# Performance work log

Measured on AMD Instinct MI355X. Metric: run time of the kernel, lower is better.

## Reference

```python
import jax, jax.numpy as jnp
import numpy as np

RBF_START = 0.0
RBF_END = 8.0
RBF_STEPS = 32
OUT_SIZE = 64
ENERGY_SCALE = 0.01


def setup_inputs() -> dict:
    key = jax.random.key(0)
    k1, k2, k3, k4 = jax.random.split(key, 4)
    L, R = 512, 4096
    return {
        "lig_feat": jax.random.normal(k1, (L, RBF_STEPS, OUT_SIZE), dtype=jnp.float32),
        "rec_feat": jax.random.normal(k2, (R, RBF_STEPS, OUT_SIZE), dtype=jnp.float32),
        "lig_coord": jax.random.normal(k3, (L, 3), dtype=jnp.float32),
        "rec_coord": jax.random.normal(k4, (R, 3), dtype=jnp.float32),
    }


def reference(lig_feat, rec_feat, lig_coord, rec_coord):
    # attention coefficients: contract over (rbf step 'e' kept, feature 'f' summed)
    atn_coefs = jnp.einsum('lef,ref->lre', lig_feat, rec_feat)  # [L,R,steps]
    # pairwise distances [L,R]
    diff = lig_coord[:, None, :] - rec_coord[None, :, :]
    dists = jnp.sqrt(jnp.sum(diff * diff, axis=-1))
    # RBF encoding [L,R,steps]
    mu = jnp.linspace(RBF_START, RBF_END, RBF_STEPS, dtype=dists.dtype)
    sigma = (RBF_START - RBF_END) / RBF_STEPS
    z = (dists[..., None] - mu) / sigma
    rbfs = jnp.exp(-(z * z))
    # weighted energy sum (scalar)
    U = jnp.sum(atn_coefs * rbfs) * ENERGY_SCALE
    return U
```

## Files before the change

### kernel.cpp

```cpp
#include <hip/hip_runtime.h>
#include <math.h>

#define LN 512
#define RN 4096
#define EN 32
#define FN 64

#define BLT 128
#define BRT 128
#define EH  8

#define K16LOG2E 23.083120654223415f
#define MU_STEP (8.0f / 31.0f)

typedef _Float16 half8 __attribute__((ext_vector_type(8)));
typedef __attribute__((ext_vector_type(4))) float f32x4;

#define APLANE 0
#define BPLANE (128 * 128)
#define LDS_BYTES (2 * 128 * 128)

__global__ __launch_bounds__(512, 1) void ff_mfma(
    const float* __restrict__ lig_feat,
    const float* __restrict__ rec_feat,
    const float* __restrict__ lig_coord,
    const float* __restrict__ rec_coord,
    float* __restrict__ partial)
{
    extern __shared__ char lds[];

    const int tid  = threadIdx.x;
    const int lane = tid & 63;
    const int w    = tid >> 6;
    const int wl   = (w & 3) * 2;
    const int wr   = (w >> 2) * 4;
    const int lrow = lane & 15;
    const int lk   = lane >> 4;

    const int l0 = blockIdx.y * BLT;
    const int r0 = blockIdx.x * BRT;
    const int e0 = blockIdx.z * EH;

    float rcx[4], rcy[4], rcz[4];
    #pragma unroll
    for (int tj = 0; tj < 4; ++tj) {
        const int r = r0 + (wr + tj) * 16 + lrow;
        rcx[tj] = rec_coord[r * 3 + 0];
        rcy[tj] = rec_coord[r * 3 + 1];
        rcz[tj] = rec_coord[r * 3 + 2];
    }
    float d[2][4][4];
    #pragma unroll
    for (int ti = 0; ti < 2; ++ti) {
        #pragma unroll
        for (int i = 0; i < 4; ++i) {
            const int l = l0 + (wl + ti) * 16 + lk * 4 + i;
            const float lx = lig_coord[l * 3 + 0];
            const float ly = lig_coord[l * 3 + 1];
            const float lz = lig_coord[l * 3 + 2];
            #pragma unroll
            for (int tj = 0; tj < 4; ++tj) {
                const float dx = lx - rcx[tj];
                const float dy = ly - rcy[tj];
                const float dz = lz - rcz[tj];
                d[ti][tj][i] = sqrtf(fmaf(dx, dx, fmaf(dy, dy, dz * dz)));
            }
        }
    }

    float usum = 0.0f;

    for (int ee = 0; ee < EH; ++ee) {
        const int e = e0 + ee;

        __syncthreads();

        #pragma unroll
        for (int k = 0; k < 8; ++k) {
            const int idx = k * 512 + tid;
            const int row = (idx >> 4) & 127;
            const int c   = idx & 15;
            const float4 v = (k < 4)
                ? *(const float4*)&lig_feat[((l0 + row) * EN + e) * FN + c * 4]
                : *(const float4*)&rec_feat[((r0 + row) * EN + e) * FN + c * 4];

            const unsigned short h0 = __builtin_bit_cast(unsigned short, (_Float16)v.x);
            const unsigned short h1 = __builtin_bit_cast(unsigned short, (_Float16)v.y);
            const unsigned short h2 = __builtin_bit_cast(unsigned short, (_Float16)v.z);
            const unsigned short h3 = __builtin_bit_cast(unsigned short, (_Float16)v.w);
            uint2 hw;
            hw.x = (unsigned)h0 | ((unsigned)h1 << 16);
            hw.y = (unsigned)h2 | ((unsigned)h3 << 16);

            const int off = row * 128 + ((c * 8) ^ ((row & 7) << 4));
            *(uint2*)(lds + ((k < 4) ? APLANE : BPLANE) + off) = hw;
        }
        __syncthreads();

        f32x4 acc[2][4];
        #pragma unroll
        for (int ti = 0; ti < 2; ++ti)
            #pragma unroll
            for (int tj = 0; tj < 4; ++tj)
                acc[ti][tj] = (f32x4){0.f, 0.f, 0.f, 0.f};

        #pragma unroll
        for (int kc = 0; kc < 2; ++kc) {
            const int inrow = (kc * 64 + lk * 16) ^ ((lrow & 7) << 4);
            half8 af[2], bf_[4];
            #pragma unroll
            for (int t = 0; t < 2; ++t) {
                const int arow = (wl + t) * 16 + lrow;
                af[t] = *(const half8*)(lds + APLANE + arow * 128 + inrow);
            }
            #pragma unroll
            for (int t = 0; t < 4; ++t) {
                const int brow = (wr + t) * 16 + lrow;
                bf_[t] = *(const half8*)(lds + BPLANE + brow * 128 + inrow);
            }
            #pragma unroll
            for (int ti = 0; ti < 2; ++ti) {
                #pragma unroll
                for (int tj = 0; tj < 4; ++tj) {
                    acc[ti][tj] = __builtin_amdgcn_mfma_f32_16x16x32_f16(
                        af[ti], bf_[tj], acc[ti][tj], 0, 0, 0);
                }
            }
        }

        const float mu = (float)e * MU_STEP;
        #pragma unroll
        for (int ti = 0; ti < 2; ++ti) {
            #pragma unroll
            for (int tj = 0; tj < 4; ++tj) {
                #pragma unroll
                for (int i = 0; i < 4; ++i) {
                    const float t = d[ti][tj][i] - mu;
                    const float wgt = __builtin_amdgcn_exp2f(-K16LOG2E * t * t);
                    usum = fmaf(acc[ti][tj][i], wgt, usum);
                }
            }
        }
    }

    __syncthreads();
    float* red = (float*)lds;
    red[tid] = usum;
    __syncthreads();
    #pragma unroll
    for (int st = 256; st > 0; st >>= 1) {
        if (tid < st) red[tid] += red[tid + st];
        __syncthreads();
    }
    if (tid == 0) {
        const int bidx = (blockIdx.z * gridDim.y + blockIdx.y) * gridDim.x + blockIdx.x;
        partial[bidx] = red[0];
    }
}

__global__ __launch_bounds__(256) void ff_reduce(
    const float* __restrict__ partial, float* __restrict__ out, int n)
{
    __shared__ float s[256];
    float v = 0.0f;
    for (int i = threadIdx.x; i < n; i += 256) v += partial[i];
    s[threadIdx.x] = v;
    __syncthreads();
    #pragma unroll
    for (int st = 128; st > 0; st >>= 1) {
        if (threadIdx.x < st) s[threadIdx.x] += s[threadIdx.x + st];
        __syncthreads();
    }
    if (threadIdx.x == 0) out[0] = s[0] * 0.01f;
}

extern "C" void kernel_launch(void* const* d_in, const int* in_sizes, int n_in,
                              void* d_out, int out_size, void* d_ws, size_t ws_size,
                              hipStream_t stream)
{
    const float* lig_feat  = (const float*)d_in[0];
    const float* rec_feat  = (const float*)d_in[1];
    const float* lig_coord = (const float*)d_in[2];
    const float* rec_coord = (const float*)d_in[3];
    float* out = (float*)d_out;
    float* partial = (float*)d_ws;

    const dim3 grid(RN / BRT, LN / BLT, EN / EH);
    ff_mfma<<<grid, dim3(512), LDS_BYTES, stream>>>(
        lig_feat, rec_feat, lig_coord, rec_coord, partial);

    const int nPartial = (RN / BRT) * (LN / BLT) * (EN / EH);
    ff_reduce<<<1, 256, 0, stream>>>(partial, out, nPartial);
}
```

Baseline: 38.93 us.

## Pre-convert features to swizzled fp16 and stream tiles via global_load_lds

Adds a separate pass that converts both feature tensors to fp16 once, stored in a swizzled per-row layout in workspace. The main kernel then fills LDS with direct global-to-LDS 16-byte loads instead of reading fp32, converting and storing in registers. This halves repeated global traffic for re-read tiles and removes the in-loop conversion work. The e-split is halved to EH=4, doubling the block count for more parallelism. In exchange it adds an extra kernel launch and a full read/write pass over the features, plus workspace usage.

```diff
diff --git a/kernel.cpp b/kernel.cpp
--- a/kernel.cpp
+++ b/kernel.cpp
@@ -8,7 +8,7 @@
 
 #define BLT 128
 #define BRT 128
-#define EH  8
+#define EH  4
 
 #define K16LOG2E 23.083120654223415f
 #define MU_STEP (8.0f / 31.0f)
@@ -20,14 +20,64 @@
 #define BPLANE (128 * 128)
 #define LDS_BYTES (2 * 128 * 128)
 
+#define WS_LIG 0
+#define WS_REC (2u * 1024 * 1024)
+#define WS_PART (18u * 1024 * 1024)
+
+#define LCHUNKS (LN * EN * 8)
+#define RCHUNKS (RN * EN * 8)
+
+typedef const __attribute__((address_space(1))) unsigned int* gas_ptr;
+typedef __attribute__((address_space(3))) unsigned int* las_ptr;
+#define GL16(g, l) __builtin_amdgcn_global_load_lds((gas_ptr)(g), (las_ptr)(l), 16, 0, 0)
+
+__global__ __launch_bounds__(256) void ff_convert(
+    const float* __restrict__ lig_feat, const float* __restrict__ rec_feat,
+    unsigned short* __restrict__ lig_swz, unsigned short* __restrict__ rec_swz)
+{
+    int idx = blockIdx.x * 256 + threadIdx.x;
+    const float* src;
+    unsigned short* dst;
+    if (idx < LCHUNKS) {
+        src = lig_feat; dst = lig_swz;
+    } else {
+        idx -= LCHUNKS;
+        src = rec_feat; dst = rec_swz;
+    }
+    const int row = idx >> 8;
+    const int e   = (idx >> 3) & 31;
+    const int gf  = idx & 7;
+
+    const float* s = src + (((size_t)row * EN + e) * FN + gf * 8);
+    const float4 v0 = *(const float4*)s;
+    const float4 v1 = *(const float4*)(s + 4);
+
+    const unsigned short q0 = __builtin_bit_cast(unsigned short, (_Float16)v0.x);
+    const unsigned short q1 = __builtin_bit_cast(unsigned short, (_Float16)v0.y);
+    const unsigned short q2 = __builtin_bit_cast(unsigned short, (_Float16)v0.z);
+    const unsigned short q3 = __builtin_bit_cast(unsigned short, (_Float16)v0.w);
+    const unsigned short q4 = __builtin_bit_cast(unsigned short, (_Float16)v1.x);
+    const unsigned short q5 = __builtin_bit_cast(unsigned short, (_Float16)v1.y);
+    const unsigned short q6 = __builtin_bit_cast(unsigned short, (_Float16)v1.z);
+    const unsigned short q7 = __builtin_bit_cast(unsigned short, (_Float16)v1.w);
+    uint4 o;
+    o.x = (unsigned)q0 | ((unsigned)q1 << 16);
+    o.y = (unsigned)q2 | ((unsigned)q3 << 16);
+    o.z = (unsigned)q4 | ((unsigned)q5 << 16);
+    o.w = (unsigned)q6 | ((unsigned)q7 << 16);
+
+    const size_t dpos = (((size_t)row * EN + e) * 8 + (gf ^ (row & 7))) * 8;
+    *(uint4*)(dst + dpos) = o;
+}
+
 __global__ __launch_bounds__(512, 1) void ff_mfma(
-    const float* __restrict__ lig_feat,
-    const float* __restrict__ rec_feat,
+    const unsigned short* __restrict__ lig_swz,
+    const unsigned short* __restrict__ rec_swz,
     const float* __restrict__ lig_coord,
     const float* __restrict__ rec_coord,
     float* __restrict__ partial)
 {
-    extern __shared__ char lds[];
+    __shared__ char lds[LDS_BYTES];
 
     const int tid  = threadIdx.x;
     const int lane = tid & 63;
@@ -41,6 +91,15 @@
     const int r0 = blockIdx.x * BRT;
     const int e0 = blockIdx.z * EH;
 
+    int soff[2];
+    #pragma unroll
+    for (int k = 0; k < 2; ++k) {
+        const int idx = k * 512 + tid;
+        soff[k] = (idx >> 3) * (EN * 128) + (idx & 7) * 16;
+    }
+    const char* ligb = (const char*)lig_swz + (size_t)l0 * (EN * 128);
+    const char* recb = (const char*)rec_swz + (size_t)r0 * (EN * 128);
+
     float rcx[4], rcy[4], rcz[4];
     #pragma unroll
     for (int tj = 0; tj < 4; ++tj) {
@@ -72,28 +131,19 @@
 
     for (int ee = 0; ee < EH; ++ee) {
         const int e = e0 + ee;
-
-        __syncthreads();
-
-        #pragma unroll
-        for (int k = 0; k < 8; ++k) {
+        const int ebyte = e * 128;
+
+        __syncthreads();
+
+        #pragma unroll
+        for (int k = 0; k < 2; ++k) {
             const int idx = k * 512 + tid;
-            const int row = (idx >> 4) & 127;
-            const int c   = idx & 15;
-            const float4 v = (k < 4)
-                ? *(const float4*)&lig_feat[((l0 + row) * EN + e) * FN + c * 4]
-                : *(const float4*)&rec_feat[((r0 + row) * EN + e) * FN + c * 4];
-
-            const unsigned short h0 = __builtin_bit_cast(unsigned short, (_Float16)v.x);
-            const unsigned short h1 = __builtin_bit_cast(unsigned short, (_Float16)v.y);
-            const unsigned short h2 = __builtin_bit_cast(unsigned short, (_Float16)v.z);
-            const unsigned short h3 = __builtin_bit_cast(unsigned short, (_Float16)v.w);
-            uint2 hw;
-            hw.x = (unsigned)h0 | ((unsigned)h1 << 16);
-            hw.y = (unsigned)h2 | ((unsigned)h3 << 16);
-
-            const int off = row * 128 + ((c * 8) ^ ((row & 7) << 4));
-            *(uint2*)(lds + ((k < 4) ? APLANE : BPLANE) + off) = hw;
+            GL16(ligb + soff[k] + ebyte, lds + APLANE + idx * 16);
+        }
+        #pragma unroll
+        for (int k = 0; k < 2; ++k) {
+            const int idx = k * 512 + tid;
+            GL16(recb + soff[k] + ebyte, lds + BPLANE + idx * 16);
         }
         __syncthreads();
 
@@ -183,11 +233,16 @@
     const float* lig_coord = (const float*)d_in[2];
     const float* rec_coord = (const float*)d_in[3];
     float* out = (float*)d_out;
-    float* partial = (float*)d_ws;
+
+    unsigned short* lig_swz = (unsigned short*)((char*)d_ws + WS_LIG);
+    unsigned short* rec_swz = (unsigned short*)((char*)d_ws + WS_REC);
+    float* partial          = (float*)((char*)d_ws + WS_PART);
+
+    const int nChunks = LCHUNKS + RCHUNKS;
+    ff_convert<<<nChunks / 256, 256, 0, stream>>>(lig_feat, rec_feat, lig_swz, rec_swz);
 
     const dim3 grid(RN / BRT, LN / BLT, EN / EH);
-    ff_mfma<<<grid, dim3(512), LDS_BYTES, stream>>>(
-        lig_feat, rec_feat, lig_coord, rec_coord, partial);
+    ff_mfma<<<grid, dim3(512), 0, stream>>>(lig_swz, rec_swz, lig_coord, rec_coord, partial);
 
     const int nPartial = (RN / BRT) * (LN / BLT) * (EN / EH);
     ff_reduce<<<1, 256, 0, stream>>>(partial, out, nPartial);
```

New measurement: 44.38 us. +14.0%, slower.
